# Kernel optimization log

Hardware: AMD Instinct MI355X
Metric: run time of the kernel (lower is better)

The kernel has to match this reference:

```python
import jax, jax.numpy as jnp
import numpy as np

B, S, E, H = 4, 2048, 1024, 16
D = E // H  # head dim


def setup_inputs() -> dict:
    key = jax.random.key(0)
    ks = jax.random.split(key, 6)
    sc = 1.0 / np.sqrt(E)
    return {
        "x":  jax.random.normal(ks[0], (B, S, E), dtype=jnp.float32),
        "Wk": jax.random.normal(ks[1], (E, E), dtype=jnp.float32) * sc,
        "Wq": jax.random.normal(ks[2], (E, E), dtype=jnp.float32) * sc,
        "Wv": jax.random.normal(ks[3], (E, E), dtype=jnp.float32) * sc,
        "Wo": jax.random.normal(ks[4], (E, E), dtype=jnp.float32) * sc,
        "bo": jax.random.normal(ks[5], (E,), dtype=jnp.float32) * sc,
    }


def reference(x, Wk, Wq, Wv, Wo, bo):
    b, s, e = x.shape
    # torch Linear: y = x @ W.T (weights are [out, in])
    K = x @ Wk.T
    Q = x @ Wq.T
    _V_unused = x @ Wv.T  # computed in source but discarded (V = Q.view bug)
    # split heads: [b, s, H, D] -> [b, H, s, D]
    Kh = K.reshape(b, s, H, D).transpose(0, 2, 1, 3)
    Qh = Q.reshape(b, s, H, D).transpose(0, 2, 1, 3)
    Vh = Qh  # faithful to source: V = Q.view(...)
    # scaled dot product, scaled by sqrt(embedding_size) as in source
    scores = jnp.einsum('bhqd,bhkd->bhqk', Qh, Kh) / jnp.sqrt(jnp.float32(e))
    causal = jnp.tril(jnp.ones((s, s), dtype=bool))
    scores = jnp.where(causal, scores, -jnp.inf)
    probs = jax.nn.softmax(scores, axis=-1)
    attn = jnp.einsum('bhqk,bhkd->bhqd', probs, Vh)
    attn = attn.transpose(0, 2, 1, 3).reshape(b, s, e)
    return attn @ Wo.T + bo
```

## Files before the change

### kernel.cpp

```cpp
#include <hip/hip_runtime.h>
#include <hip/hip_bf16.h>

#define PB 4
#define PS 2048
#define PE 1024
#define PH 16
#define PD 64

typedef __attribute__((ext_vector_type(8))) short bf16x8;
typedef __attribute__((ext_vector_type(4))) float f32x4;
typedef __attribute__((ext_vector_type(4))) unsigned int u32x4;
typedef const __attribute__((address_space(1))) unsigned int* gas_t;
typedef __attribute__((address_space(3))) unsigned int* las_t;

__device__ __forceinline__ unsigned short f2bf(float f) {
  union { float f; unsigned int u; } v;
  v.f = f;
  unsigned int u = v.u;
  u += 0x7fffu + ((u >> 16) & 1u);
  return (unsigned short)(u >> 16);
}

__device__ __forceinline__ f32x4 mfma16(bf16x8 a, bf16x8 b, f32x4 c) {
  return __builtin_amdgcn_mfma_f32_16x16x32_bf16(a, b, c, 0, 0, 0);
}

#define CVT_GROUPS ((PB * PS * PE + 3 * PE * PE) / 4)
#define CVT_BLOCKS (CVT_GROUPS / 256)
__global__ __launch_bounds__(256) void cvt_kernel(
    const float* __restrict__ x, const float* __restrict__ wk,
    const float* __restrict__ wq, const float* __restrict__ wo,
    unsigned short* __restrict__ xb, unsigned short* __restrict__ wkb,
    unsigned short* __restrict__ wqb, unsigned short* __restrict__ wob) {
  const long long NX = (long long)PB * PS * PE;
  const long long NW = (long long)PE * PE;
  long long i = ((long long)blockIdx.x * 256 + threadIdx.x) * 4;
  const float* src;
  unsigned short* dst;
  long long off;
  if (i < NX)               { src = x;  dst = xb;  off = i; }
  else if (i < NX + NW)     { src = wk; dst = wkb; off = i - NX; }
  else if (i < NX + 2 * NW) { src = wq; dst = wqb; off = i - NX - NW; }
  else                      { src = wo; dst = wob; off = i - NX - 2 * NW; }
  float4 v = *(const float4*)(src + off);
  ushort4 o;
  o.x = f2bf(v.x); o.y = f2bf(v.y); o.z = f2bf(v.z); o.w = f2bf(v.w);
  *(ushort4*)(dst + off) = o;
}

template <int MODE>
__global__ __launch_bounds__(256) void gemm_nt(
    const unsigned short* __restrict__ A, const unsigned short* __restrict__ Bm,
    const float* __restrict__ bias, float* __restrict__ Cf,
    unsigned short* __restrict__ Cb, int M, int N, int K) {
  __shared__ __attribute__((aligned(16))) unsigned short As[128 * 32];
  __shared__ __attribute__((aligned(16))) unsigned short Bs[128 * 32];
  const int tid = threadIdx.x;
  const int wave = tid >> 6, lane = tid & 63;
  const int quad = lane >> 4, ln = lane & 15;
  const int m0 = blockIdx.y * 128, n0 = blockIdx.x * 128;
  const int wm = (wave >> 1) * 64, wn = (wave & 1) * 64;
  const int sr = tid >> 2, sq = tid & 3;

  f32x4 acc[4][4];
#pragma unroll
  for (int i = 0; i < 4; ++i)
#pragma unroll
    for (int j = 0; j < 4; ++j)
#pragma unroll
      for (int r = 0; r < 4; ++r) acc[i][j][r] = 0.f;

  for (int k0 = 0; k0 < K; k0 += 32) {
    const unsigned short* ga0 = A + (size_t)(m0 + sr) * K + k0 + sq * 8;
    const unsigned short* ga1 = A + (size_t)(m0 + sr + 64) * K + k0 + sq * 8;
    const unsigned short* gb0 = Bm + (size_t)(n0 + sr) * K + k0 + sq * 8;
    const unsigned short* gb1 = Bm + (size_t)(n0 + sr + 64) * K + k0 + sq * 8;
    __builtin_amdgcn_global_load_lds((gas_t)(const void*)ga0,
        (las_t)(void*)((char*)As + tid * 16), 16, 0, 0);
    __builtin_amdgcn_global_load_lds((gas_t)(const void*)ga1,
        (las_t)(void*)((char*)As + 4096 + tid * 16), 16, 0, 0);
    __builtin_amdgcn_global_load_lds((gas_t)(const void*)gb0,
        (las_t)(void*)((char*)Bs + tid * 16), 16, 0, 0);
    __builtin_amdgcn_global_load_lds((gas_t)(const void*)gb1,
        (las_t)(void*)((char*)Bs + 4096 + tid * 16), 16, 0, 0);
    __syncthreads();
    bf16x8 af[4], bfr[4];
#pragma unroll
    for (int t = 0; t < 4; ++t) {
      af[t]  = *(const bf16x8*)(As + (wm + t * 16 + ln) * 32 + quad * 8);
      bfr[t] = *(const bf16x8*)(Bs + (wn + t * 16 + ln) * 32 + quad * 8);
    }
#pragma unroll
    for (int mt = 0; mt < 4; ++mt)
#pragma unroll
      for (int nt = 0; nt < 4; ++nt)
        acc[mt][nt] = mfma16(af[mt], bfr[nt], acc[mt][nt]);
    __syncthreads();
  }

#pragma unroll
  for (int mt = 0; mt < 4; ++mt) {
#pragma unroll
    for (int nt = 0; nt < 4; ++nt) {
      const int row = m0 + wm + mt * 16 + quad * 4;
      const int col = n0 + wn + nt * 16 + ln;
      if (MODE == 2) {
        const int b = row >> 11, s = row & 2047;
        const int h = col >> 6, d = col & 63;
        ushort4 ov;
        ov.x = f2bf(acc[mt][nt][0]); ov.y = f2bf(acc[mt][nt][1]);
        ov.z = f2bf(acc[mt][nt][2]); ov.w = f2bf(acc[mt][nt][3]);
        *(ushort4*)(Cb + (((size_t)(b * PH + h) * PD + d) * PS + s)) = ov;
      } else {
        float bv = (MODE == 0) ? bias[col] : 0.f;
#pragma unroll
        for (int r = 0; r < 4; ++r) {
          float v = acc[mt][nt][r] + bv;
          if (MODE == 0) Cf[(size_t)(row + r) * N + col] = v;
          else           Cb[(size_t)(row + r) * N + col] = f2bf(v);
        }
      }
    }
  }
}

__global__ __launch_bounds__(256) void attn_kernel(
    const unsigned short* __restrict__ QT,
    const unsigned short* __restrict__ Kb,
    unsigned short* __restrict__ Ab) {
  __shared__ __attribute__((aligned(16))) unsigned short Ks[64 * 64];
  __shared__ __attribute__((aligned(16))) unsigned short Vs[64 * 64];
  __shared__ __attribute__((aligned(16))) unsigned short Ps[4][32 * 72];

  const int tid = threadIdx.x;
  const int wave = tid >> 6, lane = tid & 63;
  const int quad = lane >> 4, ln = lane & 15;
  const int h = blockIdx.y, b = blockIdx.z;
  const size_t hoff  = ((size_t)b * PS) * PE + (size_t)h * PD;
  const size_t hofft = ((size_t)(b * PH + h) * PD) * PS;
  const float CEXP = 0.045084220f;
  const int srow = tid >> 3, sch = tid & 7;

  for (int pass = 0; pass < 2; ++pass) {
    const int qt = pass ? (int)blockIdx.x : 15 - (int)blockIdx.x;
    const int qw0 = qt * 128 + wave * 32;

    bf16x8 qfr[2][2];
#pragma unroll
    for (int nq = 0; nq < 2; ++nq)
#pragma unroll
      for (int c = 0; c < 2; ++c) {
        union { unsigned short u[8]; bf16x8 v; } tmp;
#pragma unroll
        for (int j = 0; j < 8; ++j)
          tmp.u[j] = QT[hofft + (size_t)(c * 32 + quad * 8 + j) * PS +
                        qw0 + nq * 16 + ln];
        qfr[nq][c] = tmp.v;
      }

    f32x4 o[2][4];
    float psum[2];
#pragma unroll
    for (int mq = 0; mq < 2; ++mq)
#pragma unroll
      for (int td = 0; td < 4; ++td)
#pragma unroll
        for (int r = 0; r < 4; ++r) o[mq][td][r] = 0.f;
    psum[0] = psum[1] = 0.f;

    const int ktend = 2 * qt + 2;
    for (int kt = 0; kt < ktend; ++kt) {
      const int k0 = kt * 64;

#pragma unroll
      for (int r = 0; r < 2; ++r) {
        const int row = r * 32 + srow;
        const int gch = sch ^ (row & 7);
        __builtin_amdgcn_global_load_lds(
            (gas_t)(const void*)(Kb + hoff + (size_t)(k0 + row) * PE + gch * 8),
            (las_t)(void*)((char*)Ks + (r * 256 + tid) * 16), 16, 0, 0);
        __builtin_amdgcn_global_load_lds(
            (gas_t)(const void*)(QT + hofft + (size_t)row * PS + k0 + gch * 8),
            (las_t)(void*)((char*)Vs + (r * 256 + tid) * 16), 16, 0, 0);
      }
      __syncthreads();

      f32x4 sacc[4][2];
#pragma unroll
      for (int mk = 0; mk < 4; ++mk)
#pragma unroll
        for (int nq = 0; nq < 2; ++nq)
#pragma unroll
          for (int r = 0; r < 4; ++r) sacc[mk][nq][r] = 0.f;
#pragma unroll
      for (int c = 0; c < 2; ++c) {
        const int ch = ((c * 4 + quad) ^ (ln & 7)) * 8;
        bf16x8 kf[4];
#pragma unroll
        for (int mk = 0; mk < 4; ++mk)
          kf[mk] = *(const bf16x8*)(Ks + (mk * 16 + ln) * 64 + ch);
#pragma unroll
        for (int mk = 0; mk < 4; ++mk)
#pragma unroll
          for (int nq = 0; nq < 2; ++nq)
            sacc[mk][nq] = mfma16(kf[mk], qfr[nq][c], sacc[mk][nq]);
      }

      const bool edge = (k0 + 63) > qw0;
#pragma unroll
      for (int mk = 0; mk < 4; ++mk)
#pragma unroll
        for (int nq = 0; nq < 2; ++nq) {
          float p[4];
#pragma unroll
          for (int r = 0; r < 4; ++r)
            p[r] = __builtin_amdgcn_exp2f(sacc[mk][nq][r] * CEXP);
          if (edge) {
            const int qg = qw0 + nq * 16 + ln;
#pragma unroll
            for (int r = 0; r < 4; ++r) {
              const int kg = k0 + mk * 16 + quad * 4 + r;
              p[r] = (kg <= qg) ? p[r] : 0.f;
            }
          }
          psum[nq] += (p[0] + p[1]) + (p[2] + p[3]);
          union { __hip_bfloat162 h2; unsigned int u; } u01, u23;
          u01.h2 = __float22bfloat162_rn(float2{p[0], p[1]});
          u23.h2 = __float22bfloat162_rn(float2{p[2], p[3]});
          *(uint2*)(&Ps[wave][(nq * 16 + ln) * 72 + mk * 16 + quad * 4]) =
              uint2{u01.u, u23.u};
        }

#pragma unroll
      for (int c = 0; c < 2; ++c) {
        const int ch = ((c * 4 + quad) ^ (ln & 7)) * 8;
        bf16x8 pf0 = *(const bf16x8*)(&Ps[wave][ln * 72 + c * 32 + quad * 8]);
        bf16x8 pf1 = *(const bf16x8*)(&Ps[wave][(16 + ln) * 72 + c * 32 + quad * 8]);
#pragma unroll
        for (int td = 0; td < 4; ++td) {
          bf16x8 vfd = *(const bf16x8*)(Vs + (td * 16 + ln) * 64 + ch);
          o[0][td] = mfma16(pf0, vfd, o[0][td]);
          o[1][td] = mfma16(pf1, vfd, o[1][td]);
        }
      }
      __syncthreads();
    }

#pragma unroll
    for (int nq = 0; nq < 2; ++nq) {
      psum[nq] += __shfl_xor(psum[nq], 16, 64);
      psum[nq] += __shfl_xor(psum[nq], 32, 64);
    }
    float invq[2][4];
#pragma unroll
    for (int mq = 0; mq < 2; ++mq)
#pragma unroll
      for (int r = 0; r < 4; ++r)
        invq[mq][r] = 1.f / __shfl(psum[mq], quad * 4 + r, 64);

#pragma unroll
    for (int mq = 0; mq < 2; ++mq)
#pragma unroll
      for (int r = 0; r < 4; ++r) {
        const int qg = qw0 + mq * 16 + quad * 4 + r;
#pragma unroll
        for (int td = 0; td < 4; ++td)
          Ab[hoff + (size_t)qg * PE + td * 16 + ln] =
              f2bf(o[mq][td][r] * invq[mq][r]);
      }
  }
}

extern "C" void kernel_launch(void* const* d_in, const int* in_sizes, int n_in,
                              void* d_out, int out_size, void* d_ws, size_t ws_size,
                              hipStream_t stream) {
  (void)in_sizes; (void)n_in; (void)out_size; (void)ws_size;
  const float* x  = (const float*)d_in[0];
  const float* Wk = (const float*)d_in[1];
  const float* Wq = (const float*)d_in[2];
  const float* Wo = (const float*)d_in[4];
  const float* bo = (const float*)d_in[5];
  float* out = (float*)d_out;

  char* ws = (char*)d_ws;
  unsigned short* xb  = (unsigned short*)(ws);
  unsigned short* wkb = (unsigned short*)(ws + (16u << 20));
  unsigned short* wqb = (unsigned short*)(ws + (18u << 20));
  unsigned short* wob = (unsigned short*)(ws + (20u << 20));
  unsigned short* QT  = (unsigned short*)(ws + (22u << 20));
  unsigned short* Kb  = (unsigned short*)(ws + (38u << 20));
  unsigned short* Ab  = xb;

  const int M = PB * PS;

  cvt_kernel<<<dim3(CVT_BLOCKS), dim3(256), 0, stream>>>(
      x, Wk, Wq, Wo, xb, wkb, wqb, wob);

  gemm_nt<2><<<dim3(PE / 128, M / 128), dim3(256), 0, stream>>>(
      xb, wqb, nullptr, nullptr, QT, M, PE, PE);
  gemm_nt<1><<<dim3(PE / 128, M / 128), dim3(256), 0, stream>>>(
      xb, wkb, nullptr, nullptr, Kb, M, PE, PE);

  attn_kernel<<<dim3(8, PH, PB), dim3(256), 0, stream>>>(QT, Kb, Ab);

  gemm_nt<0><<<dim3(PE / 128, M / 128), dim3(256), 0, stream>>>(
      Ab, wob, bo, out, nullptr, M, PE, PE);
}
```

Baseline: 269.2 us.

## Fuse Q and K projections into one GEMM with swizzled 64-wide K tiles

Merges the separate Q and K projection GEMMs into a single kernel that loads each x tile once and accumulates against both weight matrices, halving reads of the activation. The K tile depth doubles from 32 to 64 and an XOR swizzle is applied to the LDS layout to avoid bank conflicts on fragment reads. The output GEMM is given the same deeper, swizzled tiling. The fused kernel doubles accumulator registers (two 4x4 f32x4 sets) and uses 48KB of LDS, which may reduce occupancy.

Measured after the change: 262.0 us. 1.03x faster.

```diff
diff --git a/kernel.cpp b/kernel.cpp
--- a/kernel.cpp
+++ b/kernel.cpp
@@ -9,7 +9,6 @@
 
 typedef __attribute__((ext_vector_type(8))) short bf16x8;
 typedef __attribute__((ext_vector_type(4))) float f32x4;
-typedef __attribute__((ext_vector_type(4))) unsigned int u32x4;
 typedef const __attribute__((address_space(1))) unsigned int* gas_t;
 typedef __attribute__((address_space(3))) unsigned int* las_t;
 
@@ -48,53 +47,64 @@
   *(ushort4*)(dst + off) = o;
 }
 
-template <int MODE>
-__global__ __launch_bounds__(256) void gemm_nt(
-    const unsigned short* __restrict__ A, const unsigned short* __restrict__ Bm,
-    const float* __restrict__ bias, float* __restrict__ Cf,
-    unsigned short* __restrict__ Cb, int M, int N, int K) {
-  __shared__ __attribute__((aligned(16))) unsigned short As[128 * 32];
-  __shared__ __attribute__((aligned(16))) unsigned short Bs[128 * 32];
+__global__ __launch_bounds__(256) void gemm_qk(
+    const unsigned short* __restrict__ A, const unsigned short* __restrict__ Bq,
+    const unsigned short* __restrict__ Bk,
+    unsigned short* __restrict__ QT, unsigned short* __restrict__ Kb) {
+  const int K = PE, N = PE;
+  __shared__ __attribute__((aligned(16))) unsigned short As[128 * 64];
+  __shared__ __attribute__((aligned(16))) unsigned short Bqs[128 * 64];
+  __shared__ __attribute__((aligned(16))) unsigned short Bks[128 * 64];
   const int tid = threadIdx.x;
   const int wave = tid >> 6, lane = tid & 63;
   const int quad = lane >> 4, ln = lane & 15;
   const int m0 = blockIdx.y * 128, n0 = blockIdx.x * 128;
   const int wm = (wave >> 1) * 64, wn = (wave & 1) * 64;
-  const int sr = tid >> 2, sq = tid & 3;
-
-  f32x4 acc[4][4];
+
+  f32x4 aq[4][4], ak[4][4];
 #pragma unroll
   for (int i = 0; i < 4; ++i)
 #pragma unroll
     for (int j = 0; j < 4; ++j)
 #pragma unroll
-      for (int r = 0; r < 4; ++r) acc[i][j][r] = 0.f;
-
-  for (int k0 = 0; k0 < K; k0 += 32) {
-    const unsigned short* ga0 = A + (size_t)(m0 + sr) * K + k0 + sq * 8;
-    const unsigned short* ga1 = A + (size_t)(m0 + sr + 64) * K + k0 + sq * 8;
-    const unsigned short* gb0 = Bm + (size_t)(n0 + sr) * K + k0 + sq * 8;
-    const unsigned short* gb1 = Bm + (size_t)(n0 + sr + 64) * K + k0 + sq * 8;
-    __builtin_amdgcn_global_load_lds((gas_t)(const void*)ga0,
-        (las_t)(void*)((char*)As + tid * 16), 16, 0, 0);
-    __builtin_amdgcn_global_load_lds((gas_t)(const void*)ga1,
-        (las_t)(void*)((char*)As + 4096 + tid * 16), 16, 0, 0);
-    __builtin_amdgcn_global_load_lds((gas_t)(const void*)gb0,
-        (las_t)(void*)((char*)Bs + tid * 16), 16, 0, 0);
-    __builtin_amdgcn_global_load_lds((gas_t)(const void*)gb1,
-        (las_t)(void*)((char*)Bs + 4096 + tid * 16), 16, 0, 0);
+      for (int r = 0; r < 4; ++r) { aq[i][j][r] = 0.f; ak[i][j][r] = 0.f; }
+
+  for (int k0 = 0; k0 < K; k0 += 64) {
+#pragma unroll
+    for (int it = 0; it < 4; ++it) {
+      const int idx = it * 256 + tid;
+      const int row = idx >> 3, ch = idx & 7;
+      const int gch = ch ^ (row & 7);
+      __builtin_amdgcn_global_load_lds(
+          (gas_t)(const void*)(A + (size_t)(m0 + row) * K + k0 + gch * 8),
+          (las_t)(void*)((char*)As + idx * 16), 16, 0, 0);
+      __builtin_amdgcn_global_load_lds(
+          (gas_t)(const void*)(Bq + (size_t)(n0 + row) * K + k0 + gch * 8),
+          (las_t)(void*)((char*)Bqs + idx * 16), 16, 0, 0);
+      __builtin_amdgcn_global_load_lds(
+          (gas_t)(const void*)(Bk + (size_t)(n0 + row) * K + k0 + gch * 8),
+          (las_t)(void*)((char*)Bks + idx * 16), 16, 0, 0);
+    }
     __syncthreads();
-    bf16x8 af[4], bfr[4];
-#pragma unroll
-    for (int t = 0; t < 4; ++t) {
-      af[t]  = *(const bf16x8*)(As + (wm + t * 16 + ln) * 32 + quad * 8);
-      bfr[t] = *(const bf16x8*)(Bs + (wn + t * 16 + ln) * 32 + quad * 8);
-    }
-#pragma unroll
-    for (int mt = 0; mt < 4; ++mt)
-#pragma unroll
-      for (int nt = 0; nt < 4; ++nt)
-        acc[mt][nt] = mfma16(af[mt], bfr[nt], acc[mt][nt]);
+#pragma unroll
+    for (int kc = 0; kc < 2; ++kc) {
+      bf16x8 af[4], bqf[4], bkf[4];
+#pragma unroll
+      for (int t = 0; t < 4; ++t) {
+        const int ra = wm + t * 16 + ln;
+        const int rb = wn + t * 16 + ln;
+        af[t]  = *(const bf16x8*)(As  + ra * 64 + ((kc * 4 + quad) ^ (ra & 7)) * 8);
+        bqf[t] = *(const bf16x8*)(Bqs + rb * 64 + ((kc * 4 + quad) ^ (rb & 7)) * 8);
+        bkf[t] = *(const bf16x8*)(Bks + rb * 64 + ((kc * 4 + quad) ^ (rb & 7)) * 8);
+      }
+#pragma unroll
+      for (int mt = 0; mt < 4; ++mt)
+#pragma unroll
+        for (int nt = 0; nt < 4; ++nt) {
+          aq[mt][nt] = mfma16(af[mt], bqf[nt], aq[mt][nt]);
+          ak[mt][nt] = mfma16(af[mt], bkf[nt], ak[mt][nt]);
+        }
+    }
     __syncthreads();
   }
 
@@ -104,22 +114,82 @@
     for (int nt = 0; nt < 4; ++nt) {
       const int row = m0 + wm + mt * 16 + quad * 4;
       const int col = n0 + wn + nt * 16 + ln;
-      if (MODE == 2) {
-        const int b = row >> 11, s = row & 2047;
-        const int h = col >> 6, d = col & 63;
-        ushort4 ov;
-        ov.x = f2bf(acc[mt][nt][0]); ov.y = f2bf(acc[mt][nt][1]);
-        ov.z = f2bf(acc[mt][nt][2]); ov.w = f2bf(acc[mt][nt][3]);
-        *(ushort4*)(Cb + (((size_t)(b * PH + h) * PD + d) * PS + s)) = ov;
-      } else {
-        float bv = (MODE == 0) ? bias[col] : 0.f;
-#pragma unroll
-        for (int r = 0; r < 4; ++r) {
-          float v = acc[mt][nt][r] + bv;
-          if (MODE == 0) Cf[(size_t)(row + r) * N + col] = v;
-          else           Cb[(size_t)(row + r) * N + col] = f2bf(v);
-        }
-      }
+      const int b = row >> 11, s = row & 2047;
+      const int h = col >> 6, d = col & 63;
+      ushort4 ov;
+      ov.x = f2bf(aq[mt][nt][0]); ov.y = f2bf(aq[mt][nt][1]);
+      ov.z = f2bf(aq[mt][nt][2]); ov.w = f2bf(aq[mt][nt][3]);
+      *(ushort4*)(QT + (((size_t)(b * PH + h) * PD + d) * PS + s)) = ov;
+#pragma unroll
+      for (int r = 0; r < 4; ++r)
+        Kb[(size_t)(row + r) * N + col] = f2bf(ak[mt][nt][r]);
+    }
+  }
+}
+
+__global__ __launch_bounds__(256) void gemm_out(
+    const unsigned short* __restrict__ A, const unsigned short* __restrict__ Bm,
+    const float* __restrict__ bias, float* __restrict__ Cf) {
+  const int K = PE, N = PE;
+  __shared__ __attribute__((aligned(16))) unsigned short As[128 * 64];
+  __shared__ __attribute__((aligned(16))) unsigned short Bs[128 * 64];
+  const int tid = threadIdx.x;
+  const int wave = tid >> 6, lane = tid & 63;
+  const int quad = lane >> 4, ln = lane & 15;
+  const int m0 = blockIdx.y * 128, n0 = blockIdx.x * 128;
+  const int wm = (wave >> 1) * 64, wn = (wave & 1) * 64;
+
+  f32x4 acc[4][4];
+#pragma unroll
+  for (int i = 0; i < 4; ++i)
+#pragma unroll
+    for (int j = 0; j < 4; ++j)
+#pragma unroll
+      for (int r = 0; r < 4; ++r) acc[i][j][r] = 0.f;
+
+  for (int k0 = 0; k0 < K; k0 += 64) {
+#pragma unroll
+    for (int it = 0; it < 4; ++it) {
+      const int idx = it * 256 + tid;
+      const int row = idx >> 3, ch = idx & 7;
+      const int gch = ch ^ (row & 7);
+      __builtin_amdgcn_global_load_lds(
+          (gas_t)(const void*)(A + (size_t)(m0 + row) * K + k0 + gch * 8),
+          (las_t)(void*)((char*)As + idx * 16), 16, 0, 0);
+      __builtin_amdgcn_global_load_lds(
+          (gas_t)(const void*)(Bm + (size_t)(n0 + row) * K + k0 + gch * 8),
+          (las_t)(void*)((char*)Bs + idx * 16), 16, 0, 0);
+    }
+    __syncthreads();
+#pragma unroll
+    for (int kc = 0; kc < 2; ++kc) {
+      bf16x8 af[4], bfr[4];
+#pragma unroll
+      for (int t = 0; t < 4; ++t) {
+        const int ra = wm + t * 16 + ln;
+        const int rb = wn + t * 16 + ln;
+        af[t]  = *(const bf16x8*)(As + ra * 64 + ((kc * 4 + quad) ^ (ra & 7)) * 8);
+        bfr[t] = *(const bf16x8*)(Bs + rb * 64 + ((kc * 4 + quad) ^ (rb & 7)) * 8);
+      }
+#pragma unroll
+      for (int mt = 0; mt < 4; ++mt)
+#pragma unroll
+        for (int nt = 0; nt < 4; ++nt)
+          acc[mt][nt] = mfma16(af[mt], bfr[nt], acc[mt][nt]);
+    }
+    __syncthreads();
+  }
+
+#pragma unroll
+  for (int mt = 0; mt < 4; ++mt) {
+#pragma unroll
+    for (int nt = 0; nt < 4; ++nt) {
+      const int row = m0 + wm + mt * 16 + quad * 4;
+      const int col = n0 + wn + nt * 16 + ln;
+      const float bv = bias[col];
+#pragma unroll
+      for (int r = 0; r < 4; ++r)
+        Cf[(size_t)(row + r) * N + col] = acc[mt][nt][r] + bv;
     }
   }
 }
@@ -296,13 +366,11 @@
   cvt_kernel<<<dim3(CVT_BLOCKS), dim3(256), 0, stream>>>(
       x, Wk, Wq, Wo, xb, wkb, wqb, wob);
 
-  gemm_nt<2><<<dim3(PE / 128, M / 128), dim3(256), 0, stream>>>(
-      xb, wqb, nullptr, nullptr, QT, M, PE, PE);
-  gemm_nt<1><<<dim3(PE / 128, M / 128), dim3(256), 0, stream>>>(
-      xb, wkb, nullptr, nullptr, Kb, M, PE, PE);
+  gemm_qk<<<dim3(PE / 128, M / 128), dim3(256), 0, stream>>>(
+      xb, wqb, wkb, QT, Kb);
 
   attn_kernel<<<dim3(8, PH, PB), dim3(256), 0, stream>>>(QT, Kb, Ab);
 
-  gemm_nt<0><<<dim3(PE / 128, M / 128), dim3(256), 0, stream>>>(
-      Ab, wob, bo, out, nullptr, M, PE, PE);
-}
+  gemm_out<<<dim3(PE / 128, M / 128), dim3(256), 0, stream>>>(
+      Ab, wob, bo, out);
+}
```
